# Kernel optimization log

Measured on AMD Instinct MI355X. Metric: run time of the kernel, lower is better.

## Reference

```python
import jax, jax.numpy as jnp
import numpy as np

N_HEADS, N_LEVELS, N_POINTS = 8, 4, 4


def _bilinear(im, grid, H, W):
    # im: [N, D, H*W] flattened level feature, grid: [N, Q, P, 2] in [-1, 1]
    # F.grid_sample bilinear, padding_mode='zeros', align_corners=False
    N, Q, P, _ = grid.shape
    D = im.shape[1]
    gx = ((grid[..., 0] + 1.0) * W - 1.0) * 0.5
    gy = ((grid[..., 1] + 1.0) * H - 1.0) * 0.5
    x0f = jnp.floor(gx)
    y0f = jnp.floor(gy)
    x0 = x0f.astype(jnp.int32)
    y0 = y0f.astype(jnp.int32)
    wx1 = gx - x0f
    wy1 = gy - y0f
    acc = jnp.zeros((N, D, Q * P), im.dtype)
    corners = ((0, 0, (1 - wx1) * (1 - wy1)), (1, 0, wx1 * (1 - wy1)),
               (0, 1, (1 - wx1) * wy1), (1, 1, wx1 * wy1))
    for dx, dy, wgt in corners:
        xi = x0 + dx
        yi = y0 + dy
        valid = (xi >= 0) & (xi < W) & (yi >= 0) & (yi < H)
        idx = jnp.clip(yi, 0, H - 1) * W + jnp.clip(xi, 0, W - 1)
        v = jnp.take_along_axis(im, idx.reshape(N, 1, Q * P), axis=2)  # [N,D,QP]
        acc = acc + v * jnp.where(valid, wgt, 0.0).reshape(N, 1, Q * P)
    return acc.reshape(N, D, Q, P)


def _forward(query, value, reference_points, shapes_np,
             w_off, b_off, w_attn, b_attn, w_val, b_val, w_out, b_out):
    B, Q, E = query.shape
    H_, L, P = N_HEADS, N_LEVELS, N_POINTS
    D = E // H_
    v = (value @ w_val + b_val).reshape(B, -1, H_, D)  # [B, Nv, H, D]
    off = (query @ w_off + b_off).reshape(B, Q, H_, L, P, 2)
    attn = (query @ w_attn + b_attn).reshape(B, Q, H_, L * P)
    attn = jax.nn.softmax(attn, axis=-1).reshape(B, Q, H_, L, P)
    # offset_scale = [W_l, H_l] per level
    scale = jnp.asarray(np.stack([shapes_np[:, 1], shapes_np[:, 0]], -1), jnp.float32)
    locs = reference_points[:, :, None, :, None, :] + off / scale[None, None, None, :, None, :]
    grid = 2.0 * locs - 1.0  # [B, Q, H, L, P, 2]
    starts = np.concatenate([[0], np.cumsum(shapes_np[:, 0] * shapes_np[:, 1])]).astype(int)
    out = jnp.zeros((B * H_, D, Q), query.dtype)
    for lvl in range(L):
        h, w = int(shapes_np[lvl, 0]), int(shapes_np[lvl, 1])
        feat = v[:, starts[lvl]:starts[lvl + 1]]                      # [B, h*w, H, D]
        feat = feat.transpose(0, 2, 3, 1).reshape(B * H_, D, h * w)   # [BH, D, hw]
        g = jnp.transpose(grid[:, :, :, lvl], (0, 2, 1, 3, 4)).reshape(B * H_, Q, P, 2)
        sampled = _bilinear(feat, g, h, w)                            # [BH, D, Q, P]
        wl = jnp.transpose(attn[:, :, :, lvl], (0, 2, 1, 3)).reshape(B * H_, 1, Q, P)
        out = out + (sampled * wl).sum(-1)                            # [BH, D, Q]
    out = out.reshape(B, H_ * D, Q).transpose(0, 2, 1)                # [B, Q, E]
    return out @ w_out + b_out


def setup_inputs() -> dict:
    key = jax.random.key(0)
    ks = jax.random.split(key, 12)
    B, Q, E = 2, 19947, 256
    L, H_, P = N_LEVELS, N_HEADS, N_POINTS
    shapes = jnp.array([[100, 150], [50, 75], [25, 38], [13, 19]], dtype=jnp.int64)
    s = 0.02
    return {
        'query': jax.random.normal(ks[0], (B, Q, E), jnp.float32),
        'value': jax.random.normal(ks[1], (B, Q, E), jnp.float32),
        'reference_points': jax.random.uniform(ks[2], (B, Q, L, 2), jnp.float32),
        'spatial_shapes': shapes,
        'w_off': jax.random.normal(ks[3], (E, H_ * L * P * 2), jnp.float32) * s,
        'b_off': jax.random.normal(ks[4], (H_ * L * P * 2,), jnp.float32) * s,
        'w_attn': jax.random.normal(ks[5], (E, H_ * L * P), jnp.float32) * s,
        'b_attn': jax.random.normal(ks[6], (H_ * L * P,), jnp.float32) * s,
        'w_val': jax.random.normal(ks[7], (E, E), jnp.float32) * s,
        'b_val': jax.random.normal(ks[8], (E,), jnp.float32) * s,
        'w_out': jax.random.normal(ks[9], (E, E), jnp.float32) * s,
        'b_out': jax.random.normal(ks[10], (E,), jnp.float32) * s,
    }


def reference(query, value, reference_points, spatial_shapes,
              w_off, b_off, w_attn, b_attn, w_val, b_val, w_out, b_out):
    shapes_np = np.asarray(spatial_shapes)
    return _forward(query, value, reference_points, shapes_np,
                    w_off, b_off, w_attn, b_attn, w_val, b_val, w_out, b_out)
```

## Files before the change

### kernel.cpp

```cpp
#include <hip/hip_runtime.h>
#include <math.h>

#define B_    2
#define Q_    19947
#define E_    256
#define H_    8
#define D_    32
#define L_    4
#define P_    4

typedef _Float16 f16_t;
typedef f16_t f16x8 __attribute__((ext_vector_type(8)));
typedef f16_t f16x4 __attribute__((ext_vector_type(4)));
typedef float f32x4 __attribute__((ext_vector_type(4)));

__global__ __launch_bounds__(256)
void transpose_all(const float* __restrict__ w_val, const float* __restrict__ w_off,
                   const float* __restrict__ w_attn, const float* __restrict__ w_out,
                   f16_t* __restrict__ WtV, f16_t* __restrict__ WtQ,
                   f16_t* __restrict__ WtO)
{
    const float* in; f16_t* out; int N;
    switch (blockIdx.z) {
        case 0:  in = w_val;  out = WtV;             N = 256; break;
        case 1:  in = w_off;  out = WtQ;             N = 256; break;
        case 2:  in = w_attn; out = WtQ + 256 * 256; N = 128; break;
        default: in = w_out;  out = WtO;             N = 256; break;
    }
    const int nt = blockIdx.x * 32;
    if (nt >= N) return;
    const int kt = blockIdx.y * 32;

    __shared__ float tile[32][33];
    const int x  = threadIdx.x & 31;
    const int y0 = threadIdx.x >> 5;
    #pragma unroll
    for (int p = 0; p < 4; ++p)
        tile[y0 + p * 8][x] = in[(size_t)(kt + y0 + p * 8) * N + nt + x];
    __syncthreads();
    const int kf = kt >> 5;
    #pragma unroll
    for (int p = 0; p < 4; ++p) {
        const int n    = nt + y0 + p * 8;
        const int nf   = n >> 4, l16 = n & 15;
        const int quad = (x >> 3) & 3, e = x & 7;
        out[(size_t)(nf * 8 + kf) * 512 + (quad * 16 + l16) * 8 + e]
            = (f16_t)tile[x][y0 + p * 8];
    }
}

__global__ __launch_bounds__(256, 4)
void gemm_val(const float* __restrict__ Aval, const f16_t* __restrict__ WtV,
              const float* __restrict__ b_val,
              f16_t* __restrict__ v_proj, int M)
{
    __shared__ __align__(16) f16_t As[32][264];

    const int t  = threadIdx.x;
    const int m0 = blockIdx.x * 32;

    {
        const int r  = t >> 3;
        const int c0 = (t & 7) * 32;
        const int gm = m0 + r;
        #pragma unroll
        for (int u = 0; u < 2; ++u) {
            f16_t tmp[16];
            if (gm < M) {
                #pragma unroll
                for (int q = 0; q < 4; ++q) {
                    const float4 v4 = *(const float4*)(Aval + (size_t)gm * 256 + c0 + u * 16 + q * 4);
                    tmp[q*4+0] = (f16_t)v4.x; tmp[q*4+1] = (f16_t)v4.y;
                    tmp[q*4+2] = (f16_t)v4.z; tmp[q*4+3] = (f16_t)v4.w;
                }
            } else {
                #pragma unroll
                for (int q = 0; q < 16; ++q) tmp[q] = (f16_t)0.f;
            }
            *(f16x8*)&As[r][c0 + u * 16]     = *(const f16x8*)&tmp[0];
            *(f16x8*)&As[r][c0 + u * 16 + 8] = *(const f16x8*)&tmp[8];
        }
    }
    __syncthreads();

    const int lane = t & 63;
    const int w    = t >> 6;
    const int quad = lane >> 4, l16 = lane & 15;

    f16x8 af[2][8];
    #pragma unroll
    for (int mi = 0; mi < 2; ++mi)
        #pragma unroll
        for (int kf = 0; kf < 8; ++kf)
            af[mi][kf] = *(const f16x8*)&As[mi * 16 + l16][kf * 32 + quad * 8];

    #pragma unroll
    for (int j = 0; j < 4; ++j) {
        const int nf = w * 4 + j;
        const f16_t* __restrict__ bp = WtV + (size_t)nf * 4096 + lane * 8;

        f32x4 acc0 = {0.f, 0.f, 0.f, 0.f};
        f32x4 acc1 = {0.f, 0.f, 0.f, 0.f};
        #pragma unroll
        for (int kf = 0; kf < 8; ++kf) {
            const f16x8 bfr = *(const f16x8*)(bp + kf * 512);
            acc0 = __builtin_amdgcn_mfma_f32_16x16x32_f16(af[0][kf], bfr, acc0, 0, 0, 0);
            acc1 = __builtin_amdgcn_mfma_f32_16x16x32_f16(af[1][kf], bfr, acc1, 0, 0, 0);
        }

        const int n  = nf * 16 + l16;
        const float bv = b_val[n];
        #pragma unroll
        for (int r = 0; r < 4; ++r) {
            const int gm0 = m0 + quad * 4 + r;
            const int gm1 = gm0 + 16;
            if (gm0 < M) v_proj[(size_t)gm0 * 256 + n] = (f16_t)(acc0[r] + bv);
            if (gm1 < M) v_proj[(size_t)gm1 * 256 + n] = (f16_t)(acc1[r] + bv);
        }
    }
}

__global__ __launch_bounds__(256, 4)
void msda_fused(const f16_t* __restrict__ v,
                const float* __restrict__ Aqry,
                const f16_t* __restrict__ WtQ,
                const float* __restrict__ b_off,
                const float* __restrict__ b_attn,
                const float* __restrict__ ref,
                const f16_t* __restrict__ WoT,
                const float* __restrict__ b_out,
                float* __restrict__ out,
                int BQ)
{
    constexpr int SH[4] = {100, 50, 25, 13};
    constexpr int SW[4] = {150, 75, 38, 19};
    constexpr int ST[4] = {0, 15000, 18750, 19700};
    constexpr float LOG2E = 1.4426950408889634f;

    __shared__ __align__(16) float OffAtn[16][392];
    __shared__ __align__(16) f16_t AS[16][264];

    const int t   = threadIdx.x;
    const int bq0 = blockIdx.x * 16;

    {
        const int r  = t >> 4;
        const int c0 = (t & 15) * 16;
        const int gm = bq0 + r;
        f16_t tmp[16];
        if (gm < BQ) {
            #pragma unroll
            for (int u = 0; u < 4; ++u) {
                const float4 v4 = *(const float4*)(Aqry + (size_t)gm * 256 + c0 + u * 4);
                tmp[u*4+0] = (f16_t)v4.x; tmp[u*4+1] = (f16_t)v4.y;
                tmp[u*4+2] = (f16_t)v4.z; tmp[u*4+3] = (f16_t)v4.w;
            }
        } else {
            #pragma unroll
            for (int u = 0; u < 16; ++u) tmp[u] = (f16_t)0.f;
        }
        *(f16x8*)&AS[r][c0]     = *(const f16x8*)&tmp[0];
        *(f16x8*)&AS[r][c0 + 8] = *(const f16x8*)&tmp[8];
    }
    __syncthreads();

    {
        const int lane = t & 63;
        const int w    = t >> 6;
        const int quad = lane >> 4, l16 = lane & 15;

        f16x8 af[8];
        #pragma unroll
        for (int kf = 0; kf < 8; ++kf)
            af[kf] = *(const f16x8*)&AS[l16][kf * 32 + quad * 8];

        __builtin_amdgcn_s_setprio(1);
        #pragma unroll
        for (int j = 0; j < 6; ++j) {
            const int nf = w * 6 + j;
            const f16_t* __restrict__ bp = WtQ + (size_t)nf * 4096 + lane * 8;
            f32x4 a4 = {0.f, 0.f, 0.f, 0.f};
            #pragma unroll
            for (int kf = 0; kf < 8; ++kf) {
                const f16x8 bfr = *(const f16x8*)(bp + kf * 512);
                a4 = __builtin_amdgcn_mfma_f32_16x16x32_f16(af[kf], bfr, a4, 0, 0, 0);
            }
            const int n  = nf * 16 + l16;
            const float bv = (n < 256) ? b_off[n] : b_attn[n - 256];
            #pragma unroll
            for (int r = 0; r < 4; ++r)
                OffAtn[quad * 4 + r][n] = a4[r] + bv;
        }
        __builtin_amdgcn_s_setprio(0);
    }
    __syncthreads();

    #pragma unroll
    for (int r = 0; r < 2; ++r) {
        const int g    = t >> 2;
        const int qi   = (g >> 3) + r * 8;
        const int h    = g & 7;
        const int lane = t & 3;
        const int bq   = bq0 + qi;

        float acc[8] = {0.f, 0.f, 0.f, 0.f, 0.f, 0.f, 0.f, 0.f};

        if (bq < BQ) {
            const f16x8* __restrict__ vp = (const f16x8*)v;
            const unsigned vb = (bq >= Q_ ? (unsigned)Q_ * 32u : 0u)
                              + (unsigned)(h * 4 + lane);

            float aw[16];
            #pragma unroll
            for (int i = 0; i < 4; ++i) {
                const float4 x = *(const float4*)&OffAtn[qi][256 + h * 16 + i * 4];
                aw[i*4+0] = x.x; aw[i*4+1] = x.y; aw[i*4+2] = x.z; aw[i*4+3] = x.w;
            }
            float mx = aw[0];
            #pragma unroll
            for (int i = 1; i < 16; ++i) mx = fmaxf(mx, aw[i]);
            const float mb = mx * LOG2E;
            float sum = 0.f;
            #pragma unroll
            for (int i = 0; i < 16; ++i) {
                aw[i] = exp2f(fmaf(aw[i], LOG2E, -mb));
                sum += aw[i];
            }
            const float inv = 1.f / sum;
            #pragma unroll
            for (int i = 0; i < 16; ++i) aw[i] *= inv;

            const float4 r01 = *(const float4*)(ref + (size_t)bq * 8);
            const float4 r23 = *(const float4*)(ref + (size_t)bq * 8 + 4);
            const float rx[4] = {r01.x, r01.z, r23.x, r23.z};
            const float ry[4] = {r01.y, r01.w, r23.y, r23.w};

            #pragma unroll
            for (int l = 0; l < L_; ++l) {
                const float fW = (float)SW[l], fH = (float)SH[l];
                const int   Ww = SW[l], Hh = SH[l], st = ST[l];
                #pragma unroll
                for (int pp = 0; pp < 2; ++pp) {
                    const float4 o2 = *(const float4*)&OffAtn[qi][h * 32 + l * 8 + pp * 4];
                    #pragma unroll
                    for (int q = 0; q < 2; ++q) {
                        const int   p  = pp * 2 + q;
                        const float ox = q ? o2.z : o2.x;
                        const float oy = q ? o2.w : o2.y;
                        const float wA = aw[l * 4 + p];
                        const float gx = fmaf(rx[l], fW, ox) - 0.5f;
                        const float gy = fmaf(ry[l], fH, oy) - 0.5f;
                        const float x0f = floorf(gx), y0f = floorf(gy);
                        const int   x0  = (int)x0f,   y0  = (int)y0f;
                        const float wx1 = gx - x0f,   wy1 = gy - y0f;
                        const float wx0 = 1.f - wx1,  wy0 = 1.f - wy1;

                        const float mxw0 = ((unsigned)x0     < (unsigned)Ww) ? wx0 : 0.f;
                        const float mxw1 = ((unsigned)(x0+1) < (unsigned)Ww) ? wx1 : 0.f;
                        const float myw0 = ((unsigned)y0     < (unsigned)Hh) ? wy0 : 0.f;
                        const float myw1 = ((unsigned)(y0+1) < (unsigned)Hh) ? wy1 : 0.f;
                        const int xc0 = min(max(x0, 0),     Ww - 1);
                        const int xc1 = min(max(x0 + 1, 0), Ww - 1);
                        const int yc0 = min(max(y0, 0),     Hh - 1);
                        const int yc1 = min(max(y0 + 1, 0), Hh - 1);

                        const float w00 = wA * mxw0 * myw0;
                        const float w10 = wA * mxw1 * myw0;
                        const float w01 = wA * mxw0 * myw1;
                        const float w11 = wA * mxw1 * myw1;

                        const unsigned r0 = (unsigned)(st + yc0 * Ww);
                        const unsigned r1 = (unsigned)(st + yc1 * Ww);
                        const f16x8 s00 = vp[vb + (r0 + (unsigned)xc0) * 32u];
                        const f16x8 s10 = vp[vb + (r0 + (unsigned)xc1) * 32u];
                        const f16x8 s01 = vp[vb + (r1 + (unsigned)xc0) * 32u];
                        const f16x8 s11 = vp[vb + (r1 + (unsigned)xc1) * 32u];

                        #pragma unroll
                        for (int c = 0; c < 8; ++c) {
                            acc[c] = fmaf(w00, (float)s00[c], acc[c]);
                            acc[c] = fmaf(w10, (float)s10[c], acc[c]);
                            acc[c] = fmaf(w01, (float)s01[c], acc[c]);
                            acc[c] = fmaf(w11, (float)s11[c], acc[c]);
                        }
                    }
                }
            }
        }

        f16x8 o;
        #pragma unroll
        for (int c = 0; c < 8; ++c) o[c] = (f16_t)acc[c];
        *(f16x8*)&AS[qi][h * 32 + lane * 8] = o;
    }

    __syncthreads();

    const int lane = t & 63;
    const int w    = t >> 6;
    const int quad = lane >> 4, l16 = lane & 15;

    f16x8 af[8];
    #pragma unroll
    for (int kf = 0; kf < 8; ++kf)
        af[kf] = *(const f16x8*)&AS[l16][kf * 32 + quad * 8];

    f32x4 acc4[4];
    #pragma unroll
    for (int j = 0; j < 4; ++j) {
        f32x4 z = {0.f, 0.f, 0.f, 0.f};
        acc4[j] = z;
    }

    __builtin_amdgcn_s_setprio(1);
    #pragma unroll
    for (int j = 0; j < 4; ++j) {
        const int nf = w * 4 + j;
        const f16_t* bp = WoT + (size_t)nf * 4096 + lane * 8;
        #pragma unroll
        for (int kf = 0; kf < 8; ++kf) {
            const f16x8 bfr = *(const f16x8*)(bp + kf * 512);
            acc4[j] = __builtin_amdgcn_mfma_f32_16x16x32_f16(af[kf], bfr, acc4[j], 0, 0, 0);
        }
    }
    __builtin_amdgcn_s_setprio(0);

    #pragma unroll
    for (int j = 0; j < 4; ++j) {
        const int n  = w * 64 + j * 16 + l16;
        const float bv = b_out[n];
        #pragma unroll
        for (int r = 0; r < 4; ++r) {
            const int gm = bq0 + quad * 4 + r;
            if (gm < BQ)
                out[(size_t)gm * 256 + n] = acc4[j][r] + bv;
        }
    }
}

extern "C" void kernel_launch(void* const* d_in, const int* in_sizes, int n_in,
                              void* d_out, int out_size, void* d_ws, size_t ws_size,
                              hipStream_t stream)
{
    const float* query  = (const float*)d_in[0];
    const float* value  = (const float*)d_in[1];
    const float* refpts = (const float*)d_in[2];
    const float* w_off  = (const float*)d_in[4];
    const float* b_off  = (const float*)d_in[5];
    const float* w_attn = (const float*)d_in[6];
    const float* b_attn = (const float*)d_in[7];
    const float* w_val  = (const float*)d_in[8];
    const float* b_val  = (const float*)d_in[9];
    const float* w_out  = (const float*)d_in[10];
    const float* b_out  = (const float*)d_in[11];
    float* out = (float*)d_out;

    const int BQ = B_ * Q_;

    char* ws = (char*)d_ws;
    f16_t* v_proj = (f16_t*)ws;                       ws += (size_t)BQ * 256 * 2;
    f16_t* WtV    = (f16_t*)ws;                       ws += (size_t)256 * 256 * 2;
    f16_t* WtQ    = (f16_t*)ws;                       ws += (size_t)384 * 256 * 2;
    f16_t* WtO    = (f16_t*)ws;

    const dim3 blk(256);

    transpose_all<<<dim3(8, 8, 4), blk, 0, stream>>>(w_val, w_off, w_attn, w_out,
                                                     WtV, WtQ, WtO);

    const int mg32 = (BQ + 31) / 32;

    gemm_val<<<dim3(mg32), blk, 0, stream>>>(value, WtV, b_val, v_proj, BQ);

    const int mg16 = (BQ + 15) / 16;
    msda_fused<<<dim3(mg16), blk, 0, stream>>>(
        v_proj, query, WtQ, b_off, b_attn, refpts, WtO, b_out, out, BQ);
}
```

Baseline: 253.2 us.

## Split sampling-coordinate math across lanes and share via warp shuffles

Before, each of the 4 lanes serving a (query, head) pair recomputed the softmax and the bilinear corner indices and weights for all 16 sample points. Now each lane handles one level: it computes the softmax over 4 logits with shuffle reductions, and the corner weights and indices for its own 4 points. Those values are then broadcast to the other lanes with __shfl so each lane can still gather its own 8 channels. This removes redundant ALU work per thread at the cost of many extra shuffle instructions, and the LDS row padding also changes from 392 to 396.

Measured after the change: 254.9 us. Within noise of the previous version (+0.7%).

```diff
diff --git a/kernel.cpp b/kernel.cpp
--- a/kernel.cpp
+++ b/kernel.cpp
@@ -132,12 +132,9 @@
                 float* __restrict__ out,
                 int BQ)
 {
-    constexpr int SH[4] = {100, 50, 25, 13};
-    constexpr int SW[4] = {150, 75, 38, 19};
-    constexpr int ST[4] = {0, 15000, 18750, 19700};
     constexpr float LOG2E = 1.4426950408889634f;
 
-    __shared__ __align__(16) float OffAtn[16][392];
+    __shared__ __align__(16) float OffAtn[16][396];
     __shared__ __align__(16) f16_t AS[16][264];
 
     const int t   = threadIdx.x;
@@ -195,103 +192,111 @@
     }
     __syncthreads();
 
-    #pragma unroll
-    for (int r = 0; r < 2; ++r) {
-        const int g    = t >> 2;
-        const int qi   = (g >> 3) + r * 8;
-        const int h    = g & 7;
-        const int lane = t & 3;
-        const int bq   = bq0 + qi;
-
-        float acc[8] = {0.f, 0.f, 0.f, 0.f, 0.f, 0.f, 0.f, 0.f};
-
-        if (bq < BQ) {
-            const f16x8* __restrict__ vp = (const f16x8*)v;
-            const unsigned vb = (bq >= Q_ ? (unsigned)Q_ * 32u : 0u)
-                              + (unsigned)(h * 4 + lane);
-
-            float aw[16];
-            #pragma unroll
-            for (int i = 0; i < 4; ++i) {
-                const float4 x = *(const float4*)&OffAtn[qi][256 + h * 16 + i * 4];
-                aw[i*4+0] = x.x; aw[i*4+1] = x.y; aw[i*4+2] = x.z; aw[i*4+3] = x.w;
-            }
-            float mx = aw[0];
-            #pragma unroll
-            for (int i = 1; i < 16; ++i) mx = fmaxf(mx, aw[i]);
-            const float mb = mx * LOG2E;
-            float sum = 0.f;
-            #pragma unroll
-            for (int i = 0; i < 16; ++i) {
-                aw[i] = exp2f(fmaf(aw[i], LOG2E, -mb));
-                sum += aw[i];
-            }
-            const float inv = 1.f / sum;
-            #pragma unroll
-            for (int i = 0; i < 16; ++i) aw[i] *= inv;
-
-            const float4 r01 = *(const float4*)(ref + (size_t)bq * 8);
-            const float4 r23 = *(const float4*)(ref + (size_t)bq * 8 + 4);
-            const float rx[4] = {r01.x, r01.z, r23.x, r23.z};
-            const float ry[4] = {r01.y, r01.w, r23.y, r23.w};
-
-            #pragma unroll
-            for (int l = 0; l < L_; ++l) {
-                const float fW = (float)SW[l], fH = (float)SH[l];
-                const int   Ww = SW[l], Hh = SH[l], st = ST[l];
+    {
+        const int lv = t & 3;
+        const int   Ww = (lv==0)?150:(lv==1)?75:(lv==2)?38:19;
+        const int   Hh = (lv==0)?100:(lv==1)?50:(lv==2)?25:13;
+        const int   st = (lv==0)?0:(lv==1)?15000:(lv==2)?18750:19700;
+        const float fW = (float)Ww, fH = (float)Hh;
+
+        #pragma unroll
+        for (int r = 0; r < 2; ++r) {
+            const int g  = t >> 2;
+            const int qi = (g >> 3) + r * 8;
+            const int h  = g & 7;
+            const int bq = bq0 + qi;
+
+            float acc[8] = {0.f, 0.f, 0.f, 0.f, 0.f, 0.f, 0.f, 0.f};
+
+            if (bq < BQ) {
+                const f16x8* __restrict__ vp = (const f16x8*)v;
+                const unsigned vb = (bq >= Q_ ? (unsigned)Q_ * 32u : 0u)
+                                  + (unsigned)(h * 4 + lv);
+
+                const float4 lg = *(const float4*)&OffAtn[qi][256 + h * 16 + lv * 4];
+                float mx = fmaxf(fmaxf(lg.x, lg.y), fmaxf(lg.z, lg.w));
+                mx = fmaxf(mx, __shfl_xor(mx, 1, 4));
+                mx = fmaxf(mx, __shfl_xor(mx, 2, 4));
+                const float mb = mx * LOG2E;
+                const float e0 = exp2f(fmaf(lg.x, LOG2E, -mb));
+                const float e1 = exp2f(fmaf(lg.y, LOG2E, -mb));
+                const float e2 = exp2f(fmaf(lg.z, LOG2E, -mb));
+                const float e3 = exp2f(fmaf(lg.w, LOG2E, -mb));
+                float sum = e0 + e1 + e2 + e3;
+                sum += __shfl_xor(sum, 1, 4);
+                sum += __shfl_xor(sum, 2, 4);
+                const float inv = 1.f / sum;
+                const float a0 = e0 * inv, a1 = e1 * inv, a2 = e2 * inv, a3 = e3 * inv;
+
+                const float2 rr = *(const float2*)(ref + (size_t)bq * 8 + lv * 2);
+                const float4 oA = *(const float4*)&OffAtn[qi][h * 32 + lv * 8];
+                const float4 oB = *(const float4*)&OffAtn[qi][h * 32 + lv * 8 + 4];
+
                 #pragma unroll
-                for (int pp = 0; pp < 2; ++pp) {
-                    const float4 o2 = *(const float4*)&OffAtn[qi][h * 32 + l * 8 + pp * 4];
+                for (int p = 0; p < 4; ++p) {
+                    const float ox = (p == 0) ? oA.x : (p == 1) ? oA.z : (p == 2) ? oB.x : oB.z;
+                    const float oy = (p == 0) ? oA.y : (p == 1) ? oA.w : (p == 2) ? oB.y : oB.w;
+                    const float wA = (p == 0) ? a0 : (p == 1) ? a1 : (p == 2) ? a2 : a3;
+                    const float gx = fmaf(rr.x, fW, ox) - 0.5f;
+                    const float gy = fmaf(rr.y, fH, oy) - 0.5f;
+                    const float x0f = floorf(gx), y0f = floorf(gy);
+                    const int   x0  = (int)x0f,   y0  = (int)y0f;
+                    const float wx1 = gx - x0f,   wy1 = gy - y0f;
+                    const float wx0 = 1.f - wx1,  wy0 = 1.f - wy1;
+
+                    const float mxw0 = ((unsigned)x0     < (unsigned)Ww) ? wx0 : 0.f;
+                    const float mxw1 = ((unsigned)(x0+1) < (unsigned)Ww) ? wx1 : 0.f;
+                    const float myw0 = ((unsigned)y0     < (unsigned)Hh) ? wy0 : 0.f;
+                    const float myw1 = ((unsigned)(y0+1) < (unsigned)Hh) ? wy1 : 0.f;
+                    const int xc0 = min(max(x0, 0),     Ww - 1);
+                    const int xc1 = min(max(x0 + 1, 0), Ww - 1);
+                    const int yc0 = min(max(y0, 0),     Hh - 1);
+                    const int yc1 = min(max(y0 + 1, 0), Hh - 1);
+
+                    const float w00 = wA * mxw0 * myw0;
+                    const float w10 = wA * mxw1 * myw0;
+                    const float w01 = wA * mxw0 * myw1;
+                    const float w11 = wA * mxw1 * myw1;
+
+                    const unsigned r0 = (unsigned)(st + yc0 * Ww);
+                    const unsigned r1 = (unsigned)(st + yc1 * Ww);
+                    const unsigned i00 = r0 + (unsigned)xc0;
+                    const unsigned i10 = r0 + (unsigned)xc1;
+                    const unsigned i01 = r1 + (unsigned)xc0;
+                    const unsigned i11 = r1 + (unsigned)xc1;
+
                     #pragma unroll
-                    for (int q = 0; q < 2; ++q) {
-                        const int   p  = pp * 2 + q;
-                        const float ox = q ? o2.z : o2.x;
-                        const float oy = q ? o2.w : o2.y;
-                        const float wA = aw[l * 4 + p];
-                        const float gx = fmaf(rx[l], fW, ox) - 0.5f;
-                        const float gy = fmaf(ry[l], fH, oy) - 0.5f;
-                        const float x0f = floorf(gx), y0f = floorf(gy);
-                        const int   x0  = (int)x0f,   y0  = (int)y0f;
-                        const float wx1 = gx - x0f,   wy1 = gy - y0f;
-                        const float wx0 = 1.f - wx1,  wy0 = 1.f - wy1;
-
-                        const float mxw0 = ((unsigned)x0     < (unsigned)Ww) ? wx0 : 0.f;
-                        const float mxw1 = ((unsigned)(x0+1) < (unsigned)Ww) ? wx1 : 0.f;
-                        const float myw0 = ((unsigned)y0     < (unsigned)Hh) ? wy0 : 0.f;
-                        const float myw1 = ((unsigned)(y0+1) < (unsigned)Hh) ? wy1 : 0.f;
-                        const int xc0 = min(max(x0, 0),     Ww - 1);
-                        const int xc1 = min(max(x0 + 1, 0), Ww - 1);
-                        const int yc0 = min(max(y0, 0),     Hh - 1);
-                        const int yc1 = min(max(y0 + 1, 0), Hh - 1);
-
-                        const float w00 = wA * mxw0 * myw0;
-                        const float w10 = wA * mxw1 * myw0;
-                        const float w01 = wA * mxw0 * myw1;
-                        const float w11 = wA * mxw1 * myw1;
-
-                        const unsigned r0 = (unsigned)(st + yc0 * Ww);
-                        const unsigned r1 = (unsigned)(st + yc1 * Ww);
-                        const f16x8 s00 = vp[vb + (r0 + (unsigned)xc0) * 32u];
-                        const f16x8 s10 = vp[vb + (r0 + (unsigned)xc1) * 32u];
-                        const f16x8 s01 = vp[vb + (r1 + (unsigned)xc0) * 32u];
-                        const f16x8 s11 = vp[vb + (r1 + (unsigned)xc1) * 32u];
+                    for (int src = 0; src < 4; ++src) {
+                        const float    W00 = __shfl(w00, src, 4);
+                        const float    W10 = __shfl(w10, src, 4);
+                        const float    W01 = __shfl(w01, src, 4);
+                        const float    W11 = __shfl(w11, src, 4);
+                        const unsigned I00 = (unsigned)__shfl((int)i00, src, 4);
+                        const unsigned I10 = (unsigned)__shfl((int)i10, src, 4);
+                        const unsigned I01 = (unsigned)__shfl((int)i01, src, 4);
+                        const unsigned I11 = (unsigned)__shfl((int)i11, src, 4);
+
+                        const f16x8 s00 = vp[vb + I00 * 32u];
+                        const f16x8 s10 = vp[vb + I10 * 32u];
+                        const f16x8 s01 = vp[vb + I01 * 32u];
+                        const f16x8 s11 = vp[vb + I11 * 32u];
 
                         #pragma unroll
                         for (int c = 0; c < 8; ++c) {
-                            acc[c] = fmaf(w00, (float)s00[c], acc[c]);
-                            acc[c] = fmaf(w10, (float)s10[c], acc[c]);
-                            acc[c] = fmaf(w01, (float)s01[c], acc[c]);
-                            acc[c] = fmaf(w11, (float)s11[c], acc[c]);
+                            acc[c] = fmaf(W00, (float)s00[c], acc[c]);
+                            acc[c] = fmaf(W10, (float)s10[c], acc[c]);
+                            acc[c] = fmaf(W01, (float)s01[c], acc[c]);
+                            acc[c] = fmaf(W11, (float)s11[c], acc[c]);
                         }
                     }
                 }
             }
-        }
-
-        f16x8 o;
-        #pragma unroll
-        for (int c = 0; c < 8; ++c) o[c] = (f16_t)acc[c];
-        *(f16x8*)&AS[qi][h * 32 + lane * 8] = o;
+
+            f16x8 o;
+            #pragma unroll
+            for (int c = 0; c < 8; ++c) o[c] = (f16_t)acc[c];
+            *(f16x8*)&AS[qi][h * 32 + lv * 8] = o;
+        }
     }
 
     __syncthreads();
```
